# Performance work log

Hardware: AMD Instinct MI355X
Metric: run time of the kernel (lower is better)

The kernel has to match this reference:

```python
import jax, jax.numpy as jnp
import numpy as np

N = 50000        # nodes
E = 1_600_000    # edges (avg degree 32)
F_IN = 64        # data.num_features
H = 64           # hidden_channels
F_OUT = 1


def setup_inputs() -> dict:
    key = jax.random.key(0)
    ks = jax.random.split(key, 8)
    s = 1.0 / np.sqrt(H)  # keep activations O(1) through stacked layers
    return {
        "x": jax.random.normal(ks[0], (N, F_IN), dtype=jnp.float32),
        "edge_index": jax.random.randint(ks[1], (2, E), 0, N, dtype=jnp.int64),
        "W_in": jax.random.normal(ks[2], (F_IN, H), dtype=jnp.float32) * s,
        "b_in": jnp.zeros((H,), jnp.float32),
        "W_h1": jax.random.normal(ks[3], (H, H), dtype=jnp.float32) * s,
        "b_h1": jnp.zeros((H,), jnp.float32),
        "W_h2": jax.random.normal(ks[4], (H, H), dtype=jnp.float32) * s,
        "b_h2": jnp.zeros((H,), jnp.float32),
        "W_out": jax.random.normal(ks[5], (H, F_OUT), dtype=jnp.float32) * s,
        "b_out": jnp.zeros((F_OUT,), jnp.float32),
    }


def _gcn_conv(x, W, b, src, dst, deg_inv_sqrt, fill):
    """GCNConv: D^-1/2 (A + fill*I) D^-1/2 X W + b (PyG gcn_norm, add_self_loops)."""
    h = x @ W                                   # [N, out]
    norm = deg_inv_sqrt[src] * deg_inv_sqrt[dst]  # [E]
    agg = jnp.zeros_like(h).at[dst].add(norm[:, None] * h[src])
    # self-loop contribution with weight `fill`
    agg = agg + (fill * deg_inv_sqrt * deg_inv_sqrt)[:, None] * h
    return agg + b


def reference(x, edge_index, W_in, b_in, W_h1, b_h1, W_h2, b_h2, W_out, b_out):
    src, dst = edge_index[0], edge_index[1]
    n = x.shape[0]
    # degree at aggregation target (PyG scatter of edge weights at col)
    deg = jnp.zeros((n,), x.dtype).at[dst].add(jnp.ones((src.shape[0],), x.dtype))
    dis_improved = jax.lax.rsqrt(deg + 2.0)  # improved=True -> self-loop weight 2
    dis_plain = jax.lax.rsqrt(deg + 1.0)     # output layer: improved=False
    # dropout is identity at inference (training=False)
    h = jax.nn.relu(_gcn_conv(x, W_in, b_in, src, dst, dis_improved, 2.0))
    h = jax.nn.relu(_gcn_conv(h, W_h1, b_h1, src, dst, dis_improved, 2.0))
    h = jax.nn.relu(_gcn_conv(h, W_h2, b_h2, src, dst, dis_improved, 2.0))
    return _gcn_conv(h, W_out, b_out, src, dst, dis_plain, 1.0)
```

## Files before the change

kernel.cpp:

```cpp
#include <hip/hip_runtime.h>
#include <hip/hip_fp16.h>


#define HF 64
#define EPB 16384

__global__ __launch_bounds__(256) void pA_hist(const int* __restrict__ dst,
                                               int* __restrict__ histT, int E, int G) {
    __shared__ int h[256];
    int g = blockIdx.x, t = threadIdx.x;
    h[t] = 0;
    __syncthreads();
    int beg = g * EPB, end = min(beg + EPB, E);
    for (int i = beg + t; i < end; i += 256) atomicAdd(&h[dst[i] >> 8], 1);
    __syncthreads();
    histT[t * G + g] = h[t];
}

__global__ __launch_bounds__(128) void pScan1(int* __restrict__ hist,
                                              int* __restrict__ bsum, int G) {
    __shared__ int sd[128];
    int b = blockIdx.x, t = threadIdx.x;
    int runsum = 0;
    for (int base = 0; base < G; base += 128) {
        int idx = base + t;
        int v = (idx < G) ? hist[b * G + idx] : 0;
        sd[t] = v;
        __syncthreads();
        for (int o = 1; o < 128; o <<= 1) {
            int u = (t >= o) ? sd[t - o] : 0;
            __syncthreads();
            sd[t] += u;
            __syncthreads();
        }
        if (idx < G) hist[b * G + idx] = runsum + sd[t] - v;
        runsum += sd[127];
        __syncthreads();
    }
    if (t == 0) bsum[b] = runsum;
}

__global__ __launch_bounds__(256) void pScan2(const int* __restrict__ bsum,
                                              int* __restrict__ coarse, int E) {
    __shared__ int sd[256];
    int t = threadIdx.x;
    int v = bsum[t];
    sd[t] = v;
    __syncthreads();
    for (int o = 1; o < 256; o <<= 1) {
        int u = (t >= o) ? sd[t - o] : 0;
        __syncthreads();
        sd[t] += u;
        __syncthreads();
    }
    coarse[t] = sd[t] - v;
    if (t == 255) coarse[256] = E;
}

__global__ __launch_bounds__(256) void pB_scatter(const int* __restrict__ src,
                                                  const int* __restrict__ dst,
                                                  const int* __restrict__ histT,
                                                  const int* __restrict__ coarse,
                                                  unsigned int* __restrict__ tmp,
                                                  int E, int G) {
    __shared__ int cur[256];
    int g = blockIdx.x, t = threadIdx.x;
    cur[t] = coarse[t] + histT[t * G + g];
    __syncthreads();
    int beg = g * EPB, end = min(beg + EPB, E);
    for (int i = beg + t; i < end; i += 256) {
        int d = dst[i], s = src[i];
        int pos = atomicAdd(&cur[d >> 8], 1);
        tmp[pos] = ((unsigned int)(d & 255) << 16) | (unsigned int)(s & 0xFFFF);
    }
}

__global__ __launch_bounds__(256) void pC_build(const unsigned int* __restrict__ tmp,
                                                const int* __restrict__ coarse,
                                                ushort* __restrict__ csrs,
                                                int* __restrict__ offs,
                                                float* __restrict__ di,
                                                float* __restrict__ dp,
                                                int n, int E, int NB) {
    __shared__ int hist[256];
    __shared__ int cur[256];
    __shared__ int scanbuf[256];
    int b = blockIdx.x, t = threadIdx.x;
    int beg = coarse[b], end = coarse[b + 1];
    hist[t] = 0;
    __syncthreads();
    for (int i = beg + t; i < end; i += 256) atomicAdd(&hist[tmp[i] >> 16], 1);
    __syncthreads();
    int v = hist[t];
    scanbuf[t] = v;
    __syncthreads();
    for (int o = 1; o < 256; o <<= 1) {
        int u = (t >= o) ? scanbuf[t - o] : 0;
        __syncthreads();
        scanbuf[t] += u;
        __syncthreads();
    }
    int excl = scanbuf[t] - v;
    cur[t] = beg + excl;
    int d = (b << 8) + t;
    if (d < n) {
        offs[d] = beg + excl;
        float df = (float)v;
        di[d] = rsqrtf(df + 2.0f);
        dp[d] = rsqrtf(df + 1.0f);
    }
    if (b == NB - 1 && t == 0) offs[n] = E;
    __syncthreads();
    for (int i = beg + t; i < end; i += 256) {
        unsigned int e = tmp[i];
        int pos = atomicAdd(&cur[e >> 16], 1);
        csrs[pos] = (ushort)(e & 0xFFFFu);
    }
}

#define GM_BN 128
__global__ __launch_bounds__(256) void k_gemm(const float* __restrict__ A,
                                              const float* __restrict__ W,
                                              const float* __restrict__ di,
                                              __half* __restrict__ C, int n) {
    __shared__ float xT[64][132];
    __shared__ float Wl[64][64];
    int tid = threadIdx.x;
    int nb = blockIdx.x * GM_BN;

    for (int r = 0; r < 4; ++r) {
        int q = tid + 256 * r;
        int row = q >> 4, c4 = (q & 15) << 2;
        *(float4*)&Wl[row][c4] = *(const float4*)&W[row * 64 + c4];
    }
    for (int r = 0; r < 8; ++r) {
        int q = tid + 256 * r;
        int nl = q >> 4, k0 = (q & 15) << 2;
        float4 v = make_float4(0.f, 0.f, 0.f, 0.f);
        if (nb + nl < n) v = *(const float4*)&A[(size_t)(nb + nl) * HF + k0];
        xT[k0 + 0][nl] = v.x; xT[k0 + 1][nl] = v.y;
        xT[k0 + 2][nl] = v.z; xT[k0 + 3][nl] = v.w;
    }
    __syncthreads();

    int tx = tid & 7;
    int ty = tid >> 3;
    int f0 = tx * 8, n0 = ty * 4;
    float acc[4][8];
#pragma unroll
    for (int i = 0; i < 4; ++i)
#pragma unroll
        for (int j = 0; j < 8; ++j) acc[i][j] = 0.f;

#pragma unroll 4
    for (int k = 0; k < 64; ++k) {
        float4 xa = *(float4*)&xT[k][n0];
        float4 wa = *(float4*)&Wl[k][f0];
        float4 wb = *(float4*)&Wl[k][f0 + 4];
        float xs[4] = {xa.x, xa.y, xa.z, xa.w};
        float wsv[8] = {wa.x, wa.y, wa.z, wa.w, wb.x, wb.y, wb.z, wb.w};
#pragma unroll
        for (int i = 0; i < 4; ++i)
#pragma unroll
            for (int j = 0; j < 8; ++j) acc[i][j] += xs[i] * wsv[j];
    }

#pragma unroll
    for (int i = 0; i < 4; ++i) {
        int nn = nb + n0 + i;
        if (nn < n) {
            float dr = di[nn];
            union { __half h[8]; float4 f4; } u;
#pragma unroll
            for (int j = 0; j < 8; ++j) u.h[j] = __float2half(acc[i][j] * dr);
            *(float4*)&C[(size_t)nn * HF + f0] = u.f4;
        }
    }
}

__device__ __forceinline__ void agg_edges2(const __half2* __restrict__ P2,
                                           const ushort* __restrict__ csrs,
                                           int beg, int deg, int half, int fh,
                                           float& A0, float& A1) {
    float a0 = 0.f, a1 = 0.f;
    int pairs = deg >> 1;
    int e = beg + half;
    int chunks = pairs >> 1;
    for (int c = 0; c < chunks; ++c, e += 4) {
        int s0 = csrs[e];
        int s1 = csrs[e + 2];
        float2 v0 = __half22float2(P2[(size_t)s0 * 32 + fh]);
        float2 v1 = __half22float2(P2[(size_t)s1 * 32 + fh]);
        a0 += v0.x; a1 += v0.y;
        a0 += v1.x; a1 += v1.y;
    }
    if (pairs & 1) {
        int s = csrs[e];
        float2 v = __half22float2(P2[(size_t)s * 32 + fh]);
        a0 += v.x; a1 += v.y;
    }
    if ((deg & 1) && half == 0) {
        int s = csrs[beg + deg - 1];
        float2 v = __half22float2(P2[(size_t)s * 32 + fh]);
        a0 += v.x; a1 += v.y;
    }
    a0 += __shfl_xor(a0, 32);
    a1 += __shfl_xor(a1, 32);
    A0 = a0; A1 = a1;
}

__global__ __launch_bounds__(256) void k_agg(const __half2* __restrict__ P2,
                      const int* __restrict__ offs, const ushort* __restrict__ csrs,
                      const float* __restrict__ di, const float* __restrict__ bias,
                      float* __restrict__ out, int n, float fill) {
    int wid = (blockIdx.x * blockDim.x + threadIdx.x) >> 6;
    if (wid >= n) return;
    int lane = threadIdx.x & 63;
    int half = lane >> 5, fh = lane & 31;
    int beg = offs[wid], deg = offs[wid + 1] - beg;
    float a0, a1;
    agg_edges2(P2, csrs, beg, deg, half, fh, a0, a1);
    float dw = di[wid];
    float2 self = __half22float2(P2[(size_t)wid * 32 + fh]);
    a0 = fmaxf(dw * (a0 + fill * self.x) + bias[2 * fh + 0], 0.f);
    a1 = fmaxf(dw * (a1 + fill * self.y) + bias[2 * fh + 1], 0.f);
    if (half == 0) {
        float* op = &out[(size_t)wid * HF + 2 * fh];
        __builtin_nontemporal_store(a0, op);
        __builtin_nontemporal_store(a1, op + 1);
    }
}

__global__ __launch_bounds__(256) void k_agg_final(const __half2* __restrict__ P2,
                      const int* __restrict__ offs, const ushort* __restrict__ csrs,
                      const float* __restrict__ di, const float* __restrict__ bias,
                      const float* __restrict__ Wout, const float* __restrict__ dp,
                      float* __restrict__ z2, int n) {
    int wid = (blockIdx.x * blockDim.x + threadIdx.x) >> 6;
    if (wid >= n) return;
    int lane = threadIdx.x & 63;
    int half = lane >> 5, fh = lane & 31;
    int beg = offs[wid], deg = offs[wid + 1] - beg;
    float a0, a1;
    agg_edges2(P2, csrs, beg, deg, half, fh, a0, a1);
    float dw = di[wid];
    float2 self = __half22float2(P2[(size_t)wid * 32 + fh]);
    a0 = fmaxf(dw * (a0 + 2.0f * self.x) + bias[2 * fh + 0], 0.f);
    a1 = fmaxf(dw * (a1 + 2.0f * self.y) + bias[2 * fh + 1], 0.f);
    float v = a0 * Wout[2 * fh] + a1 * Wout[2 * fh + 1];
#pragma unroll
    for (int o = 16; o > 0; o >>= 1) v += __shfl_down(v, o, 32);
    if (lane == 0) z2[wid] = v * dp[wid];
}

__global__ void k_out(const float* __restrict__ z2, const int* __restrict__ offs,
                      const ushort* __restrict__ csrs, const float* __restrict__ dp,
                      const float* __restrict__ bout, float* __restrict__ out, int n) {
    int i = blockIdx.x * blockDim.x + threadIdx.x;
    if (i >= n) return;
    int beg = offs[i], end = offs[i + 1];
    float acc = 0.f;
    for (int e = beg; e < end; ++e) acc += z2[csrs[e]];
    out[i] = dp[i] * (acc + z2[i]) + bout[0];
}

extern "C" void kernel_launch(void* const* d_in, const int* in_sizes, int n_in,
                              void* d_out, int out_size, void* d_ws, size_t ws_size,
                              hipStream_t stream) {
    const float* x    = (const float*)d_in[0];
    const int*   ei   = (const int*)d_in[1];
    const float* W_in = (const float*)d_in[2];
    const float* b_in = (const float*)d_in[3];
    const float* W_h1 = (const float*)d_in[4];
    const float* b_h1 = (const float*)d_in[5];
    const float* W_h2 = (const float*)d_in[6];
    const float* b_h2 = (const float*)d_in[7];
    const float* W_out= (const float*)d_in[8];
    const float* b_out= (const float*)d_in[9];
    float* out = (float*)d_out;

    const int n = in_sizes[0] / HF;
    const int E = in_sizes[1] / 2;
    const int* src = ei;
    const int* dst = ei + E;

    const int G  = (E + EPB - 1) / EPB;
    const int NB = (n + 255) >> 8;

    char* ws = (char*)d_ws;
    size_t o = 0;
    auto alloc = [&](size_t bytes) -> void* {
        void* p = ws + o;
        o += (bytes + 255) & ~(size_t)255;
        return p;
    };
    int*          offs   = (int*)   alloc((size_t)(n + 1) * 4);
    float*        di     = (float*) alloc((size_t)n * 4);
    float*        dp     = (float*) alloc((size_t)n * 4);
    ushort*       csrs   = (ushort*)alloc((size_t)E * 2);
    unsigned int* tmp    = (unsigned int*)alloc((size_t)E * 4);
    int*          histT  = (int*)   alloc((size_t)G * 256 * 4);
    int*          bsum   = (int*)   alloc(256 * 4);
    int*          coarse = (int*)   alloc(257 * 4);
    __half*       hW     = (__half*)alloc((size_t)n * HF * 2);
    float*        hA     = (float*) alloc((size_t)n * HF * 4);
    float*        hB     = (float*) alloc((size_t)n * HF * 4);
    float*        z2     = (float*) alloc((size_t)n * 4);

    const int TB = 256;
    int gbN = (n + TB - 1) / TB;
    int gbW = (n * 64 + TB - 1) / TB;
    int gbG = (n + GM_BN - 1) / GM_BN;

    pA_hist   <<<G,   TB, 0, stream>>>(dst, histT, E, G);
    pScan1    <<<256, 128, 0, stream>>>(histT, bsum, G);
    pScan2    <<<1,   TB, 0, stream>>>(bsum, coarse, E);
    pB_scatter<<<G,   TB, 0, stream>>>(src, dst, histT, coarse, tmp, E, G);
    pC_build  <<<NB,  TB, 0, stream>>>(tmp, coarse, csrs, offs, di, dp, n, E, NB);

    const __half2* hW2 = (const __half2*)hW;

    k_gemm<<<gbG, TB, 0, stream>>>(x, W_in, di, hW, n);
    k_agg<<<gbW, TB, 0, stream>>>(hW2, offs, csrs, di, b_in, hA, n, 2.0f);
    k_gemm<<<gbG, TB, 0, stream>>>(hA, W_h1, di, hW, n);
    k_agg<<<gbW, TB, 0, stream>>>(hW2, offs, csrs, di, b_h1, hB, n, 2.0f);
    k_gemm<<<gbG, TB, 0, stream>>>(hB, W_h2, di, hW, n);
    k_agg_final<<<gbW, TB, 0, stream>>>(hW2, offs, csrs, di, b_h2, W_out, dp, z2, n);
    k_out<<<gbN, TB, 0, stream>>>(z2, offs, csrs, dp, b_out, out, n);
}
```

Measured before the change: 277.7 us.

## Partition CSR by source slice for L2-local gathers, then reduce partials

The edge sort key becomes (source quarter, destination), producing four CSR slices. Each aggregation layer now runs a scatter kernel in which blocks are mapped to one source slice, so the gathered rows form a smaller working set that may stay in a cache or XCD-local L2. This is followed by a reduce kernel that sums the four fp16 partials and applies normalization, bias and ReLU. Degree computation moves to a separate kernel, and the output kernel switches to 16 lanes per node. The cost is extra partial-buffer traffic, fp16 rounding of the partials, and additional kernel launches.

```diff
diff --git a/kernel.cpp b/kernel.cpp
--- a/kernel.cpp
+++ b/kernel.cpp
@@ -5,14 +5,21 @@
 #define HF 64
 #define EPB 16384
 
-__global__ __launch_bounds__(256) void pA_hist(const int* __restrict__ dst,
-                                               int* __restrict__ histT, int E, int G) {
+__global__ __launch_bounds__(256) void pA_hist(const int* __restrict__ src,
+                                               const int* __restrict__ dst,
+                                               int* __restrict__ histT,
+                                               int E, int G, int n, int q) {
     __shared__ int h[256];
     int g = blockIdx.x, t = threadIdx.x;
     h[t] = 0;
     __syncthreads();
     int beg = g * EPB, end = min(beg + EPB, E);
-    for (int i = beg + t; i < end; i += 256) atomicAdd(&h[dst[i] >> 8], 1);
+    for (int i = beg + t; i < end; i += 256) {
+        int s = src[i], d = dst[i];
+        int slice = (s >= 3 * q) ? 3 : (s >= 2 * q) ? 2 : (s >= q) ? 1 : 0;
+        int key = slice * n + d;
+        atomicAdd(&h[key >> 10], 1);
+    }
     __syncthreads();
     histT[t * G + g] = h[t];
 }
@@ -62,59 +69,77 @@
                                                   const int* __restrict__ histT,
                                                   const int* __restrict__ coarse,
                                                   unsigned int* __restrict__ tmp,
-                                                  int E, int G) {
+                                                  int E, int G, int n, int q) {
     __shared__ int cur[256];
     int g = blockIdx.x, t = threadIdx.x;
     cur[t] = coarse[t] + histT[t * G + g];
     __syncthreads();
     int beg = g * EPB, end = min(beg + EPB, E);
     for (int i = beg + t; i < end; i += 256) {
-        int d = dst[i], s = src[i];
-        int pos = atomicAdd(&cur[d >> 8], 1);
-        tmp[pos] = ((unsigned int)(d & 255) << 16) | (unsigned int)(s & 0xFFFF);
+        int s = src[i], d = dst[i];
+        int slice = (s >= 3 * q) ? 3 : (s >= 2 * q) ? 2 : (s >= q) ? 1 : 0;
+        int key = slice * n + d;
+        int pos = atomicAdd(&cur[key >> 10], 1);
+        tmp[pos] = ((unsigned int)(key & 1023) << 16) | (unsigned int)(s & 0xFFFF);
     }
 }
 
 __global__ __launch_bounds__(256) void pC_build(const unsigned int* __restrict__ tmp,
                                                 const int* __restrict__ coarse,
                                                 ushort* __restrict__ csrs,
-                                                int* __restrict__ offs,
-                                                float* __restrict__ di,
-                                                float* __restrict__ dp,
-                                                int n, int E, int NB) {
-    __shared__ int hist[256];
-    __shared__ int cur[256];
-    __shared__ int scanbuf[256];
+                                                int* __restrict__ offs4,
+                                                int n4, int E, int NB2) {
+    __shared__ int hist[1024];
+    __shared__ int cur[1024];
+    __shared__ int tsum[256];
     int b = blockIdx.x, t = threadIdx.x;
     int beg = coarse[b], end = coarse[b + 1];
-    hist[t] = 0;
+#pragma unroll
+    for (int j = 0; j < 4; ++j) hist[4 * t + j] = 0;
     __syncthreads();
     for (int i = beg + t; i < end; i += 256) atomicAdd(&hist[tmp[i] >> 16], 1);
     __syncthreads();
-    int v = hist[t];
-    scanbuf[t] = v;
+    int h0 = hist[4 * t], h1 = hist[4 * t + 1], h2 = hist[4 * t + 2], h3 = hist[4 * t + 3];
+    int s = h0 + h1 + h2 + h3;
+    tsum[t] = s;
     __syncthreads();
     for (int o = 1; o < 256; o <<= 1) {
-        int u = (t >= o) ? scanbuf[t - o] : 0;
-        __syncthreads();
-        scanbuf[t] += u;
-        __syncthreads();
-    }
-    int excl = scanbuf[t] - v;
-    cur[t] = beg + excl;
-    int d = (b << 8) + t;
-    if (d < n) {
-        offs[d] = beg + excl;
-        float df = (float)v;
-        di[d] = rsqrtf(df + 2.0f);
-        dp[d] = rsqrtf(df + 1.0f);
-    }
-    if (b == NB - 1 && t == 0) offs[n] = E;
+        int u = (t >= o) ? tsum[t - o] : 0;
+        __syncthreads();
+        tsum[t] += u;
+        __syncthreads();
+    }
+    int b0 = beg + tsum[t] - s;
+    cur[4 * t + 0] = b0;
+    cur[4 * t + 1] = b0 + h0;
+    cur[4 * t + 2] = b0 + h0 + h1;
+    cur[4 * t + 3] = b0 + h0 + h1 + h2;
+    int keybase = (b << 10) + 4 * t;
+#pragma unroll
+    for (int j = 0; j < 4; ++j) {
+        int key = keybase + j;
+        if (key < n4) offs4[key] = cur[4 * t + j];
+    }
+    if (b == NB2 - 1 && t == 0) offs4[n4] = E;
     __syncthreads();
     for (int i = beg + t; i < end; i += 256) {
         unsigned int e = tmp[i];
         int pos = atomicAdd(&cur[e >> 16], 1);
         csrs[pos] = (ushort)(e & 0xFFFFu);
+    }
+}
+
+__global__ void k_dis(const int* __restrict__ offs4, float* __restrict__ di,
+                      float* __restrict__ dp, int n) {
+    int i = blockIdx.x * blockDim.x + threadIdx.x;
+    if (i < n) {
+        int deg = 0;
+#pragma unroll
+        for (int s = 0; s < 4; ++s)
+            deg += offs4[(size_t)s * n + i + 1] - offs4[(size_t)s * n + i];
+        float df = (float)deg;
+        di[i] = rsqrtf(df + 2.0f);
+        dp[i] = rsqrtf(df + 1.0f);
     }
 }
 
@@ -178,90 +203,117 @@
     }
 }
 
-__device__ __forceinline__ void agg_edges2(const __half2* __restrict__ P2,
-                                           const ushort* __restrict__ csrs,
-                                           int beg, int deg, int half, int fh,
-                                           float& A0, float& A1) {
-    float a0 = 0.f, a1 = 0.f;
-    int pairs = deg >> 1;
-    int e = beg + half;
-    int chunks = pairs >> 1;
-    for (int c = 0; c < chunks; ++c, e += 4) {
-        int s0 = csrs[e];
-        int s1 = csrs[e + 2];
-        float2 v0 = __half22float2(P2[(size_t)s0 * 32 + fh]);
-        float2 v1 = __half22float2(P2[(size_t)s1 * 32 + fh]);
-        a0 += v0.x; a1 += v0.y;
-        a0 += v1.x; a1 += v1.y;
-    }
-    if (pairs & 1) {
-        int s = csrs[e];
-        float2 v = __half22float2(P2[(size_t)s * 32 + fh]);
-        a0 += v.x; a1 += v.y;
-    }
-    if ((deg & 1) && half == 0) {
-        int s = csrs[beg + deg - 1];
-        float2 v = __half22float2(P2[(size_t)s * 32 + fh]);
-        a0 += v.x; a1 += v.y;
-    }
-    a0 += __shfl_xor(a0, 32);
-    a1 += __shfl_xor(a1, 32);
-    A0 = a0; A1 = a1;
-}
-
-__global__ __launch_bounds__(256) void k_agg(const __half2* __restrict__ P2,
-                      const int* __restrict__ offs, const ushort* __restrict__ csrs,
-                      const float* __restrict__ di, const float* __restrict__ bias,
-                      float* __restrict__ out, int n, float fill) {
-    int wid = (blockIdx.x * blockDim.x + threadIdx.x) >> 6;
-    if (wid >= n) return;
+__global__ __launch_bounds__(256) void k_scat(const __half2* __restrict__ P2,
+                                              const int* __restrict__ offs4,
+                                              const ushort* __restrict__ csrs,
+                                              __half2* __restrict__ part, int n) {
+    int bid = blockIdx.x;
+    int c = (bid & 7) >> 1;
+    int rank = ((bid >> 3) << 1) | (bid & 1);
+    int wrank = rank * 4 + (threadIdx.x >> 6);
     int lane = threadIdx.x & 63;
     int half = lane >> 5, fh = lane & 31;
-    int beg = offs[wid], deg = offs[wid + 1] - beg;
-    float a0, a1;
-    agg_edges2(P2, csrs, beg, deg, half, fh, a0, a1);
-    float dw = di[wid];
-    float2 self = __half22float2(P2[(size_t)wid * 32 + fh]);
-    a0 = fmaxf(dw * (a0 + fill * self.x) + bias[2 * fh + 0], 0.f);
-    a1 = fmaxf(dw * (a1 + fill * self.y) + bias[2 * fh + 1], 0.f);
-    if (half == 0) {
-        float* op = &out[(size_t)wid * HF + 2 * fh];
-        __builtin_nontemporal_store(a0, op);
-        __builtin_nontemporal_store(a1, op + 1);
-    }
-}
-
-__global__ __launch_bounds__(256) void k_agg_final(const __half2* __restrict__ P2,
-                      const int* __restrict__ offs, const ushort* __restrict__ csrs,
-                      const float* __restrict__ di, const float* __restrict__ bias,
-                      const float* __restrict__ Wout, const float* __restrict__ dp,
-                      float* __restrict__ z2, int n) {
-    int wid = (blockIdx.x * blockDim.x + threadIdx.x) >> 6;
-    if (wid >= n) return;
-    int lane = threadIdx.x & 63;
-    int half = lane >> 5, fh = lane & 31;
-    int beg = offs[wid], deg = offs[wid + 1] - beg;
-    float a0, a1;
-    agg_edges2(P2, csrs, beg, deg, half, fh, a0, a1);
-    float dw = di[wid];
-    float2 self = __half22float2(P2[(size_t)wid * 32 + fh]);
-    a0 = fmaxf(dw * (a0 + 2.0f * self.x) + bias[2 * fh + 0], 0.f);
-    a1 = fmaxf(dw * (a1 + 2.0f * self.y) + bias[2 * fh + 1], 0.f);
-    float v = a0 * Wout[2 * fh] + a1 * Wout[2 * fh + 1];
+    const int* offc = offs4 + (size_t)c * n;
+    __half2* pc = part + (size_t)c * n * 32;
+    for (int node = wrank; node < n; node += 2048) {
+        int beg = offc[node], deg = offc[node + 1] - beg;
+        float a0 = 0.f, a1 = 0.f;
+        int pairs = deg >> 1;
+        int e = beg + half;
+        int c2 = pairs >> 1;
+        for (int i2 = 0; i2 < c2; ++i2, e += 4) {
+            int s0 = csrs[e], s1 = csrs[e + 2];
+            float2 v0 = __half22float2(P2[(size_t)s0 * 32 + fh]);
+            float2 v1 = __half22float2(P2[(size_t)s1 * 32 + fh]);
+            a0 += v0.x; a1 += v0.y;
+            a0 += v1.x; a1 += v1.y;
+        }
+        if (pairs & 1) {
+            int s0 = csrs[e];
+            float2 v = __half22float2(P2[(size_t)s0 * 32 + fh]);
+            a0 += v.x; a1 += v.y;
+        }
+        if ((deg & 1) && half == 0) {
+            int s0 = csrs[beg + deg - 1];
+            float2 v = __half22float2(P2[(size_t)s0 * 32 + fh]);
+            a0 += v.x; a1 += v.y;
+        }
+        a0 += __shfl_xor(a0, 32);
+        a1 += __shfl_xor(a1, 32);
+        if (half == 0) {
+            __half2 hv = __floats2half2_rn(a0, a1);
+            unsigned uv = *(unsigned*)&hv;
+            __builtin_nontemporal_store(uv, (unsigned*)(pc + (size_t)node * 32 + fh));
+        }
+    }
+}
+
+__global__ __launch_bounds__(256) void k_reduce(const __half2* __restrict__ part,
+                                                const __half2* __restrict__ P2,
+                                                const float* __restrict__ di,
+                                                const float* __restrict__ bias,
+                                                float* __restrict__ out, int n,
+                                                float fill) {
+    int idx = blockIdx.x * 256 + threadIdx.x;
+    int node = idx >> 5, fh = idx & 31;
+    if (node >= n) return;
+    float a0 = 0.f, a1 = 0.f;
+#pragma unroll
+    for (int s = 0; s < 4; ++s) {
+        float2 v = __half22float2(part[((size_t)s * n + node) * 32 + fh]);
+        a0 += v.x; a1 += v.y;
+    }
+    float dw = di[node];
+    float2 self = __half22float2(P2[(size_t)node * 32 + fh]);
+    float h0 = fmaxf(dw * (a0 + fill * self.x) + bias[2 * fh + 0], 0.f);
+    float h1 = fmaxf(dw * (a1 + fill * self.y) + bias[2 * fh + 1], 0.f);
+    float* op = &out[(size_t)node * HF + 2 * fh];
+    __builtin_nontemporal_store(h0, op);
+    __builtin_nontemporal_store(h1, op + 1);
+}
+
+__global__ __launch_bounds__(256) void k_reduce_final(const __half2* __restrict__ part,
+                                                      const __half2* __restrict__ P2,
+                                                      const float* __restrict__ di,
+                                                      const float* __restrict__ bias,
+                                                      const float* __restrict__ Wout,
+                                                      const float* __restrict__ dp,
+                                                      float* __restrict__ z2, int n) {
+    int idx = blockIdx.x * 256 + threadIdx.x;
+    int node = idx >> 5, fh = idx & 31;
+    if (node >= n) return;
+    float a0 = 0.f, a1 = 0.f;
+#pragma unroll
+    for (int s = 0; s < 4; ++s) {
+        float2 v = __half22float2(part[((size_t)s * n + node) * 32 + fh]);
+        a0 += v.x; a1 += v.y;
+    }
+    float dw = di[node];
+    float2 self = __half22float2(P2[(size_t)node * 32 + fh]);
+    float h0 = fmaxf(dw * (a0 + 2.0f * self.x) + bias[2 * fh + 0], 0.f);
+    float h1 = fmaxf(dw * (a1 + 2.0f * self.y) + bias[2 * fh + 1], 0.f);
+    float v = h0 * Wout[2 * fh] + h1 * Wout[2 * fh + 1];
 #pragma unroll
     for (int o = 16; o > 0; o >>= 1) v += __shfl_down(v, o, 32);
-    if (lane == 0) z2[wid] = v * dp[wid];
-}
-
-__global__ void k_out(const float* __restrict__ z2, const int* __restrict__ offs,
-                      const ushort* __restrict__ csrs, const float* __restrict__ dp,
-                      const float* __restrict__ bout, float* __restrict__ out, int n) {
-    int i = blockIdx.x * blockDim.x + threadIdx.x;
-    if (i >= n) return;
-    int beg = offs[i], end = offs[i + 1];
+    if ((threadIdx.x & 31) == 0) z2[node] = v * dp[node];
+}
+
+__global__ __launch_bounds__(256) void k_out(const float* __restrict__ z2,
+                      const int* __restrict__ offs4, const ushort* __restrict__ csrs,
+                      const float* __restrict__ dp, const float* __restrict__ bout,
+                      float* __restrict__ out, int n) {
+    int node = (blockIdx.x * blockDim.x + threadIdx.x) >> 4;
+    if (node >= n) return;
+    int l = threadIdx.x & 15;
     float acc = 0.f;
-    for (int e = beg; e < end; ++e) acc += z2[csrs[e]];
-    out[i] = dp[i] * (acc + z2[i]) + bout[0];
+#pragma unroll
+    for (int s = 0; s < 4; ++s) {
+        int beg = offs4[(size_t)s * n + node], end = offs4[(size_t)s * n + node + 1];
+        for (int e = beg + l; e < end; e += 16) acc += z2[csrs[e]];
+    }
+#pragma unroll
+    for (int o = 8; o > 0; o >>= 1) acc += __shfl_down(acc, o, 16);
+    if (l == 0) out[node] = dp[node] * (acc + z2[node]) + bout[0];
 }
 
 extern "C" void kernel_launch(void* const* d_in, const int* in_sizes, int n_in,
@@ -284,8 +336,10 @@
     const int* src = ei;
     const int* dst = ei + E;
 
-    const int G  = (E + EPB - 1) / EPB;
-    const int NB = (n + 255) >> 8;
+    const int q   = (n + 3) >> 2;
+    const int n4  = 4 * n;
+    const int G   = (E + EPB - 1) / EPB;
+    const int NB2 = (n4 + 1023) >> 10;
 
     char* ws = (char*)d_ws;
     size_t o = 0;
@@ -294,7 +348,7 @@
         o += (bytes + 255) & ~(size_t)255;
         return p;
     };
-    int*          offs   = (int*)   alloc((size_t)(n + 1) * 4);
+    int*          offs4  = (int*)   alloc((size_t)(n4 + 1) * 4);
     float*        di     = (float*) alloc((size_t)n * 4);
     float*        dp     = (float*) alloc((size_t)n * 4);
     ushort*       csrs   = (ushort*)alloc((size_t)E * 2);
@@ -303,28 +357,34 @@
     int*          bsum   = (int*)   alloc(256 * 4);
     int*          coarse = (int*)   alloc(257 * 4);
     __half*       hW     = (__half*)alloc((size_t)n * HF * 2);
+    __half2*      part   = (__half2*)alloc((size_t)4 * n * 32 * 4);
     float*        hA     = (float*) alloc((size_t)n * HF * 4);
     float*        hB     = (float*) alloc((size_t)n * HF * 4);
     float*        z2     = (float*) alloc((size_t)n * 4);
 
     const int TB = 256;
-    int gbN = (n + TB - 1) / TB;
-    int gbW = (n * 64 + TB - 1) / TB;
-    int gbG = (n + GM_BN - 1) / GM_BN;
-
-    pA_hist   <<<G,   TB, 0, stream>>>(dst, histT, E, G);
+    int gbDis = (n + TB - 1) / TB;
+    int gbR   = (n * 32 + TB - 1) / TB;
+    int gbO   = (n * 16 + TB - 1) / TB;
+    int gbG   = (n + GM_BN - 1) / GM_BN;
+
+    pA_hist   <<<G,   TB, 0, stream>>>(src, dst, histT, E, G, n, q);
     pScan1    <<<256, 128, 0, stream>>>(histT, bsum, G);
     pScan2    <<<1,   TB, 0, stream>>>(bsum, coarse, E);
-    pB_scatter<<<G,   TB, 0, stream>>>(src, dst, histT, coarse, tmp, E, G);
-    pC_build  <<<NB,  TB, 0, stream>>>(tmp, coarse, csrs, offs, di, dp, n, E, NB);
+    pB_scatter<<<G,   TB, 0, stream>>>(src, dst, histT, coarse, tmp, E, G, n, q);
+    pC_build  <<<NB2, TB, 0, stream>>>(tmp, coarse, csrs, offs4, n4, E, NB2);
+    k_dis     <<<gbDis, TB, 0, stream>>>(offs4, di, dp, n);
 
     const __half2* hW2 = (const __half2*)hW;
 
-    k_gemm<<<gbG, TB, 0, stream>>>(x, W_in, di, hW, n);
-    k_agg<<<gbW, TB, 0, stream>>>(hW2, offs, csrs, di, b_in, hA, n, 2.0f);
-    k_gemm<<<gbG, TB, 0, stream>>>(hA, W_h1, di, hW, n);
-    k_agg<<<gbW, TB, 0, stream>>>(hW2, offs, csrs, di, b_h1, hB, n, 2.0f);
-    k_gemm<<<gbG, TB, 0, stream>>>(hB, W_h2, di, hW, n);
-    k_agg_final<<<gbW, TB, 0, stream>>>(hW2, offs, csrs, di, b_h2, W_out, dp, z2, n);
-    k_out<<<gbN, TB, 0, stream>>>(z2, offs, csrs, dp, b_out, out, n);
-}
+    k_gemm  <<<gbG,  TB, 0, stream>>>(x, W_in, di, hW, n);
+    k_scat  <<<2048, TB, 0, stream>>>(hW2, offs4, csrs, part, n);
+    k_reduce<<<gbR,  TB, 0, stream>>>(part, hW2, di, b_in, hA, n, 2.0f);
+    k_gemm  <<<gbG,  TB, 0, stream>>>(hA, W_h1, di, hW, n);
+    k_scat  <<<2048, TB, 0, stream>>>(hW2, offs4, csrs, part, n);
+    k_reduce<<<gbR,  TB, 0, stream>>>(part, hW2, di, b_h1, hB, n, 2.0f);
+    k_gemm        <<<gbG,  TB, 0, stream>>>(hB, W_h2, di, hW, n);
+    k_scat        <<<2048, TB, 0, stream>>>(hW2, offs4, csrs, part, n);
+    k_reduce_final<<<gbR,  TB, 0, stream>>>(part, hW2, di, b_h2, W_out, dp, z2, n);
+    k_out<<<gbO, TB, 0, stream>>>(z2, offs4, csrs, dp, b_out, out, n);
+}
```

New measurement: 282.7 us. Within noise of the previous version (+1.8%).
